# Kernel optimization log

Hardware: AMD Instinct MI355X
Metric: run time of the kernel (lower is better)

## Reference

```python
import jax, jax.numpy as jnp
import numpy as np

B, N, DIM = 8, 256, 256
INTER = DIM // 4          # downsample=4
POS_H = 64                # pos_mlp_hidden_dim
ATTN_H = INTER * 4        # attn_mlp_hidden_mult=4


def setup_inputs() -> dict:
    key = jax.random.key(0)
    ks = jax.random.split(key, 16)
    s = lambda fan_in: 1.0 / np.sqrt(fan_in)
    return {
        "x": jax.random.normal(ks[0], (B, N, DIM), jnp.float32),
        "y": jax.random.normal(ks[1], (B, N, DIM), jnp.float32),
        "x_pos": jax.random.normal(ks[2], (B, N, 3), jnp.float32),
        "y_pos": jax.random.normal(ks[3], (B, N, 3), jnp.float32),
        "mask": jax.random.randint(ks[4], (B, N), 0, 2) > 0,
        # linear weights stored (in, out) for direct matmul; torch Linear has no bias for g/theta/phi/conv_out
        "g_w": jax.random.normal(ks[5], (DIM, INTER), jnp.float32) * s(DIM),
        "theta_w": jax.random.normal(ks[6], (DIM, INTER), jnp.float32) * s(DIM),
        "phi_w": jax.random.normal(ks[7], (DIM, INTER), jnp.float32) * s(DIM),
        "pos_w1": jax.random.normal(ks[8], (3, POS_H), jnp.float32) * s(3),
        "pos_b1": jnp.zeros((POS_H,), jnp.float32),
        "pos_w2": jax.random.normal(ks[9], (POS_H, INTER), jnp.float32) * s(POS_H),
        "pos_b2": jnp.zeros((INTER,), jnp.float32),
        "attn_w1": jax.random.normal(ks[10], (INTER, ATTN_H), jnp.float32) * s(INTER),
        "attn_b1": jnp.zeros((ATTN_H,), jnp.float32),
        "attn_w2": jax.random.normal(ks[11], (ATTN_H, INTER), jnp.float32) * s(ATTN_H),
        "attn_b2": jnp.zeros((INTER,), jnp.float32),
        "out_w": jax.random.normal(ks[12], (INTER, DIM), jnp.float32) * s(INTER),
    }


def reference(x, y, x_pos, y_pos, mask, g_w, theta_w, phi_w,
              pos_w1, pos_b1, pos_w2, pos_b2,
              attn_w1, attn_b1, attn_w2, attn_b2, out_w):
    v = y @ g_w            # (b, j, d)
    q = x @ theta_w        # (b, i, d)
    k = y @ phi_w          # (b, j, d)
    # pairwise relative positions -> MLP embedding, (b, i, j, d)
    rel_pos = x_pos[:, :, None, :] - y_pos[:, None, :, :]
    rel_pos_emb = jax.nn.relu(rel_pos @ pos_w1 + pos_b1) @ pos_w2 + pos_b2
    # MLP-based attention score on (q_i - k_j + rel_pos_emb)
    qk_rel = q[:, :, None, :] - k[:, None, :, :]
    sim = jax.nn.relu((qk_rel + rel_pos_emb) @ attn_w1 + attn_b1) @ attn_w2 + attn_b2
    # masked softmax over j (dim=-2)
    pair_mask = mask[:, :, None] & mask[:, None, :]      # (b, i, j)
    neg = -jnp.finfo(sim.dtype).max
    sim = jnp.where(pair_mask[..., None], sim, neg)
    attn = jax.nn.softmax(sim, axis=-2)
    # value + positional embedding, then per-channel weighted aggregate over j
    v_full = v[:, None, :, :] + rel_pos_emb              # (b, i, j, d)
    agg = jnp.einsum('bijd,bijd->bid', attn, v_full)
    return x + agg @ out_w
```

## Files before the change

kernel.cpp:

```cpp
#include <hip/hip_runtime.h>
#include <hip/hip_bf16.h>

#define NB 8
#define NN 256
#define DIMV 256
#define DI 64
#define NEGMAX 3.402823466e+38f

typedef unsigned short u16;
typedef unsigned int u32;
typedef __attribute__((ext_vector_type(8))) short bf16x8;
typedef __attribute__((ext_vector_type(4))) float f32x4;
typedef __attribute__((ext_vector_type(2))) float f32x2;
typedef __attribute__((ext_vector_type(2))) unsigned int u32x2;

__device__ __forceinline__ u16 f2bf(float f) {
    __hip_bfloat16 h = __float2bfloat16(f);
    u16 u; __builtin_memcpy(&u, &h, 2); return u;
}
__device__ __forceinline__ u32 pack2(float a, float b) {
    return (u32)f2bf(a) | ((u32)f2bf(b) << 16);
}
__device__ __forceinline__ float ubf_lo(u32 u) {
    union { u32 u; float f; } x; x.u = u << 16; return x.f;
}
__device__ __forceinline__ float ubf_hi(u32 u) {
    union { u32 u; float f; } x; x.u = u & 0xffff0000u; return x.f;
}
__device__ __forceinline__ int fA(int row) { return ((row & 7) << 4) ^ ((row & 8) << 2); }
__device__ __forceinline__ int fB(int row) { return ((row >> 1) & 7) << 4; }

__global__ void prep_all(const float* __restrict__ x, const float* __restrict__ y,
                         const float* __restrict__ tw, const float* __restrict__ pw,
                         const float* __restrict__ gw,
                         const float* __restrict__ w1, const float* __restrict__ w2,
                         const float* __restrict__ pw2,
                         const float* __restrict__ pw1, const float* __restrict__ pb1,
                         float* __restrict__ q, float* __restrict__ k, float* __restrict__ v,
                         u16* __restrict__ w1s, u16* __restrict__ w2s,
                         u16* __restrict__ pw2s, u16* __restrict__ pw1f)
{
    __shared__ float xs[4][256];
    __shared__ float ys[4][256];
    const int blk = blockIdx.x;
    const int tid = threadIdx.x;

    if (blk >= 512) {
        const int idx = (blk - 512) * 256 + tid;
        const int e   = idx & 7;
        const int l   = (idx >> 3) & 63;
        const int l15 = l & 15, lh = l >> 4;
        {
            const int frag = idx >> 9;
            const int ks = frag & 1, c2 = (frag >> 1) & 1, hc = frag >> 2;
            w1s[idx] = f2bf(w1[(ks * 32 + lh * 8 + e) * 256 + hc * 32 + 2 * l15 + c2]);
        }
        {
            const int frag = idx >> 9;
            const int ct = frag & 3, hc = frag >> 2;
            w2s[idx] = f2bf(w2[(hc * 32 + lh * 8 + e) * 64 + 4 * l15 + ct]);
        }
        if (idx < 4096) {
            const int frag = idx >> 9;
            const int ks = frag & 1, ct = frag >> 1;
            pw2s[idx] = f2bf(pw2[(ks * 32 + lh * 8 + e) * 64 + 4 * l15 + ct]);
        }
        if (idx < 2048) {
            const int ct = idx >> 9;
            const int kk = lh * 8 + e;
            const int col = 4 * l15 + ct;
            float val = (kk < 3) ? pw1[kk * 64 + col] : ((kk == 3) ? pb1[col] : 0.f);
            pw1f[idx] = f2bf(val);
        }
        return;
    }

    const int b = blk >> 6;
    const int n0 = (blk & 63) * 4;
    {
        int r = tid >> 6, e = tid & 63;
        ((float4*)xs[r])[e] = ((const float4*)(x + (size_t)(b * NN + n0 + r) * DIMV))[e];
        ((float4*)ys[r])[e] = ((const float4*)(y + (size_t)(b * NN + n0 + r) * DIMV))[e];
    }
    __syncthreads();
    const int nl = tid >> 6, d = tid & 63;
    float aq = 0.f, ak = 0.f, av = 0.f;
    #pragma unroll 4
    for (int c = 0; c < 256; ++c) {
        float wq = tw[c * 64 + d], wk = pw[c * 64 + d], wv = gw[c * 64 + d];
        float xv = xs[nl][c], yv = ys[nl][c];
        aq += xv * wq; ak += yv * wk; av += yv * wv;
    }
    const int n = n0 + nl;
    q[(b * NN + n) * DI + d] = aq;
    k[(b * NN + n) * DI + d] = ak;
    v[(b * NN + n) * DI + d] = av;
}

__global__ __launch_bounds__(256, 2)
void fused_attn(const float* __restrict__ x, const float* __restrict__ x_pos,
                const float* __restrict__ y_pos, const int* __restrict__ mask,
                const float* __restrict__ pb2,
                const float* __restrict__ ab1, const float* __restrict__ ab2,
                const float* __restrict__ out_w,
                const float* __restrict__ qg, const float* __restrict__ kg,
                const float* __restrict__ vg,
                const u16* __restrict__ w1s, const u16* __restrict__ w2s,
                const u16* __restrict__ pw2s, const u16* __restrict__ pw1f,
                float* __restrict__ out)
{
    __shared__ __align__(16) char sT[4][8192];
    __shared__ __align__(16) char sHid[4][4096];
    __shared__ __align__(16) char sV2[4][4096];

    const int blk = blockIdx.x;
    const int b = blk >> 8;
    const int i = blk & 255;
    const int tid = threadIdx.x;
    const int l   = tid & 63;
    const int w   = tid >> 6;
    const int j0  = w * 64;
    const int l15 = l & 15;
    const int lh  = l >> 4;

    char* const sTw   = sT[w];
    char* const sHidw = sHid[w];
    char* const sV2w  = sV2[w];

    int stW[4], hcW[4];
    #pragma unroll
    for (int r = 0; r < 4; ++r) {
        const int lr = lh * 4 + r;
        stW[r] = (lr * 128 + l15 * 8) ^ fA(lr);
        hcW[r] = (lr * 64 + l15 * 4) ^ fB(lr);
    }
    const int stR0 = (l15 * 128 + lh * 16) ^ fA(l15);
    const int stR1 = stR0 ^ 64;
    const int hcR  = (l15 * 64 + lh * 16) ^ fB(l15);

    const int mjl = mask[b * NN + j0 + l];
    const unsigned long long mb = __ballot(mjl != 0);
    const bool mi_b = mask[b * NN + i] != 0;

    const float xp0 = x_pos[(b * NN + i) * 3 + 0];
    const float xp1 = x_pos[(b * NN + i) * 3 + 1];
    const float xp2 = x_pos[(b * NN + i) * 3 + 2];

    bf16x8 afr[4];
    #pragma unroll
    for (int rt = 0; rt < 4; ++rt) {
        const float* yp = y_pos + (size_t)(b * NN + j0 + rt * 16 + l15) * 3;
        const float r0 = xp0 - yp[0], r1 = xp1 - yp[1], r2 = xp2 - yp[2];
        union { u32 u[4]; bf16x8 v; } c;
        c.u[0] = (lh == 0) ? pack2(r0, r1) : 0u;
        c.u[1] = (lh == 0) ? pack2(r2, 1.0f) : 0u;
        c.u[2] = 0u; c.u[3] = 0u;
        afr[rt] = c.v;
    }
    bf16x8 pw1b[4];
    #pragma unroll
    for (int ct = 0; ct < 4; ++ct)
        pw1b[ct] = *(const bf16x8*)(pw1f + (ct * 64 + l) * 8);

    const f32x4 qv   = *(const f32x4*)&qg[((size_t)b * NN + i) * DI + 4 * l15];
    const f32x4 pb2v = *(const f32x4*)&pb2[4 * l15];
    bf16x8 bfr[4][2];
    #pragma unroll
    for (int ct = 0; ct < 4; ++ct)
        #pragma unroll
        for (int ks = 0; ks < 2; ++ks)
            bfr[ct][ks] = *(const bf16x8*)(pw2s + ((ct * 2 + ks) * 64 + l) * 8);

    f32x4 hA[4];
    #define HID_MFMA(RT)                                                        \
        { _Pragma("unroll") for (int ct = 0; ct < 4; ++ct) {                    \
            f32x4 z = {0.f, 0.f, 0.f, 0.f};                                     \
            hA[ct] = __builtin_amdgcn_mfma_f32_16x16x32_bf16(afr[RT], pw1b[ct], z, 0, 0, 0); } }
    #define HID_STORE(RT)                                                       \
        { char* hb = sHidw + (((RT) & 1) ? 2048 : 0);                           \
          _Pragma("unroll") for (int r = 0; r < 4; ++r) {                       \
            u32x2 hpk;                                                          \
            hpk[0] = pack2(fmaxf(hA[0][r], 0.f), fmaxf(hA[1][r], 0.f));         \
            hpk[1] = pack2(fmaxf(hA[2][r], 0.f), fmaxf(hA[3][r], 0.f));         \
            *(u32x2*)(hb + stW[r]) = hpk; } }

    u32x2 accVp[2][4];
    HID_MFMA(0);
    HID_STORE(0);
    #pragma unroll
    for (int rt = 0; rt < 4; ++rt) {
        if (rt < 3) { HID_MFMA(rt + 1); HID_STORE(rt + 1); }
        char* const hb = sHidw + ((rt & 1) ? 2048 : 0);
        const bf16x8 afc0 = *(const bf16x8*)(hb + stR0);
        const bf16x8 afc1 = *(const bf16x8*)(hb + stR1);

        f32x4 accR[4];
        #pragma unroll
        for (int ct = 0; ct < 4; ++ct) {
            f32x4 a = {pb2v[ct], pb2v[ct], pb2v[ct], pb2v[ct]};
            a = __builtin_amdgcn_mfma_f32_16x16x32_bf16(afc0, bfr[ct][0], a, 0, 0, 0);
            a = __builtin_amdgcn_mfma_f32_16x16x32_bf16(afc1, bfr[ct][1], a, 0, 0, 0);
            accR[ct] = a;
        }
        #pragma unroll
        for (int r = 0; r < 4; ++r) {
            const int row = j0 + rt * 16 + lh * 4 + r;
            const f32x4 kv = *(const f32x4*)&kg[((size_t)b * NN + row) * DI + 4 * l15];
            const f32x4 vv = *(const f32x4*)&vg[((size_t)b * NN + row) * DI + 4 * l15];
            float tv[4], vf[4];
            #pragma unroll
            for (int ct = 0; ct < 4; ++ct) {
                const float rpe = accR[ct][r];
                tv[ct] = qv[ct] - kv[ct] + rpe;
                vf[ct] = vv[ct] + rpe;
            }
            u32x2 tpk; tpk[0] = pack2(tv[0], tv[1]); tpk[1] = pack2(tv[2], tv[3]);
            u32x2 vpk; vpk[0] = pack2(vf[0], vf[1]); vpk[1] = pack2(vf[2], vf[3]);
            *(u32x2*)(sTw + stW[r] + rt * 2048) = tpk;
            if (rt < 2) accVp[rt][r] = vpk;
            else        *(u32x2*)(sV2w + stW[r] + (rt - 2) * 2048) = vpk;
        }
    }

    bf16x8 aT[4][2];
    #pragma unroll
    for (int rt = 0; rt < 4; ++rt) {
        aT[rt][0] = *(const bf16x8*)(sTw + stR0 + rt * 2048);
        aT[rt][1] = *(const bf16x8*)(sTw + stR1 + rt * 2048);
    }

    const f32x4 ab2v = *(const f32x4*)&ab2[4 * l15];
    f32x4 accS[4][4];
    #pragma unroll
    for (int rt = 0; rt < 4; ++rt)
        #pragma unroll
        for (int ct = 0; ct < 4; ++ct)
            accS[rt][ct] = (f32x4){ab2v[ct], ab2v[ct], ab2v[ct], ab2v[ct]};

    #pragma unroll
    for (int hc = 0; hc < 8; ++hc) {
        bf16x8 b1f[2][2];
        #pragma unroll
        for (int c2 = 0; c2 < 2; ++c2)
            #pragma unroll
            for (int ks = 0; ks < 2; ++ks)
                b1f[c2][ks] = *(const bf16x8*)(w1s + ((hc * 4 + c2 * 2 + ks) * 64 + l) * 8);
        bf16x8 b2f[4];
        #pragma unroll
        for (int ct = 0; ct < 4; ++ct)
            b2f[ct] = *(const bf16x8*)(w2s + ((hc * 4 + ct) * 64 + l) * 8);
        const f32x2 ab1v = *(const f32x2*)&ab1[hc * 32 + 2 * l15];
        const f32x4 ib0 = {ab1v[0], ab1v[0], ab1v[0], ab1v[0]};
        const f32x4 ib1 = {ab1v[1], ab1v[1], ab1v[1], ab1v[1]};
        __builtin_amdgcn_s_setprio(1);
        #pragma unroll
        for (int rt = 0; rt < 4; ++rt) {
            f32x4 h0 = ib0, h1 = ib1;
            h0 = __builtin_amdgcn_mfma_f32_16x16x32_bf16(aT[rt][0], b1f[0][0], h0, 0, 0, 0);
            h0 = __builtin_amdgcn_mfma_f32_16x16x32_bf16(aT[rt][1], b1f[0][1], h0, 0, 0, 0);
            h1 = __builtin_amdgcn_mfma_f32_16x16x32_bf16(aT[rt][0], b1f[1][0], h1, 0, 0, 0);
            h1 = __builtin_amdgcn_mfma_f32_16x16x32_bf16(aT[rt][1], b1f[1][1], h1, 0, 0, 0);
            #pragma unroll
            for (int r = 0; r < 4; ++r)
                *(u32*)(sHidw + hcW[r] + rt * 1024) =
                    pack2(fmaxf(h0[r], 0.f), fmaxf(h1[r], 0.f));
        }
        bf16x8 a2[4];
        #pragma unroll
        for (int rt = 0; rt < 4; ++rt)
            a2[rt] = *(const bf16x8*)(sHidw + hcR + rt * 1024);
        #pragma unroll
        for (int rt = 0; rt < 4; ++rt)
            #pragma unroll
            for (int ct = 0; ct < 4; ++ct)
                accS[rt][ct] = __builtin_amdgcn_mfma_f32_16x16x32_bf16(a2[rt], b2f[ct], accS[rt][ct], 0, 0, 0);
        __builtin_amdgcn_s_setprio(0);
    }

    float mx[4] = {-NEGMAX, -NEGMAX, -NEGMAX, -NEGMAX};
    #pragma unroll
    for (int rt = 0; rt < 4; ++rt)
        #pragma unroll
        for (int r = 0; r < 4; ++r) {
            const int ro = rt * 16 + lh * 4 + r;
            const bool bit = mi_b && ((mb >> ro) & 1ull);
            #pragma unroll
            for (int ct = 0; ct < 4; ++ct) {
                float s = bit ? accS[rt][ct][r] : -NEGMAX;
                accS[rt][ct][r] = s;
                mx[ct] = fmaxf(mx[ct], s);
            }
        }
    #pragma unroll
    for (int ct = 0; ct < 4; ++ct) {
        mx[ct] = fmaxf(mx[ct], __shfl_xor(mx[ct], 16));
        mx[ct] = fmaxf(mx[ct], __shfl_xor(mx[ct], 32));
    }
    float ssum[4] = {0.f, 0.f, 0.f, 0.f}, sagg[4] = {0.f, 0.f, 0.f, 0.f};
    #pragma unroll
    for (int rt = 0; rt < 4; ++rt)
        #pragma unroll
        for (int r = 0; r < 4; ++r) {
            u32x2 vpk;
            if (rt < 2) vpk = accVp[rt][r];
            else        vpk = *(const u32x2*)(sV2w + stW[r] + (rt - 2) * 2048);
            const float vfs[4] = {ubf_lo(vpk[0]), ubf_hi(vpk[0]), ubf_lo(vpk[1]), ubf_hi(vpk[1])};
            #pragma unroll
            for (int ct = 0; ct < 4; ++ct) {
                const float e = __expf(accS[rt][ct][r] - mx[ct]);
                ssum[ct] += e;
                sagg[ct] += e * vfs[ct];
            }
        }
    #pragma unroll
    for (int ct = 0; ct < 4; ++ct) {
        ssum[ct] += __shfl_xor(ssum[ct], 16);
        ssum[ct] += __shfl_xor(ssum[ct], 32);
        sagg[ct] += __shfl_xor(sagg[ct], 16);
        sagg[ct] += __shfl_xor(sagg[ct], 32);
    }
    {
        float* const redW = (float*)&sHid[w][0];
        if (lh == 0) {
            *(f32x4*)&redW[      4 * l15] = (f32x4){mx[0], mx[1], mx[2], mx[3]};
            *(f32x4*)&redW[ 64 + 4 * l15] = (f32x4){ssum[0], ssum[1], ssum[2], ssum[3]};
            *(f32x4*)&redW[128 + 4 * l15] = (f32x4){sagg[0], sagg[1], sagg[2], sagg[3]};
        }
    }
    __syncthreads();
    float* const redAll = (float*)&sHid[0][0];
    if (tid < 64) {
        const float m0 = redAll[tid],        m1 = redAll[1024 + tid],
                    m2 = redAll[2048 + tid], m3 = redAll[3072 + tid];
        const float M = fmaxf(fmaxf(m0, m1), fmaxf(m2, m3));
        const float e0 = __expf(m0 - M), e1 = __expf(m1 - M),
                    e2 = __expf(m2 - M), e3 = __expf(m3 - M);
        const float den = redAll[64 + tid] * e0 + redAll[1024 + 64 + tid] * e1
                        + redAll[2048 + 64 + tid] * e2 + redAll[3072 + 64 + tid] * e3;
        const float num = redAll[128 + tid] * e0 + redAll[1024 + 128 + tid] * e1
                        + redAll[2048 + 128 + tid] * e2 + redAll[3072 + 128 + tid] * e3;
        redAll[192 + tid] = num / den;
    }
    __syncthreads();

    {
        float acc = 0.f;
        #pragma unroll 16
        for (int d = 0; d < 64; ++d)
            acc += redAll[192 + d] * out_w[d * DIMV + tid];
        const int o = (b * NN + i) * DIMV + tid;
        out[o] = x[o] + acc;
    }
}

extern "C" void kernel_launch(void* const* d_in, const int* in_sizes, int n_in,
                              void* d_out, int out_size, void* d_ws, size_t ws_size,
                              hipStream_t stream)
{
    const float* x       = (const float*)d_in[0];
    const float* y       = (const float*)d_in[1];
    const float* x_pos   = (const float*)d_in[2];
    const float* y_pos   = (const float*)d_in[3];
    const int*   mask    = (const int*)d_in[4];
    const float* g_w     = (const float*)d_in[5];
    const float* theta_w = (const float*)d_in[6];
    const float* phi_w   = (const float*)d_in[7];
    const float* pos_w1  = (const float*)d_in[8];
    const float* pos_b1  = (const float*)d_in[9];
    const float* pos_w2  = (const float*)d_in[10];
    const float* pos_b2  = (const float*)d_in[11];
    const float* attn_w1 = (const float*)d_in[12];
    const float* attn_b1 = (const float*)d_in[13];
    const float* attn_w2 = (const float*)d_in[14];
    const float* attn_b2 = (const float*)d_in[15];
    const float* out_w   = (const float*)d_in[16];

    float* q = (float*)d_ws;
    float* k = q + NB * NN * DI;
    float* v = k + NB * NN * DI;
    u16* w1s  = (u16*)(v + NB * NN * DI);
    u16* w2s  = w1s + 16384;
    u16* pw2s = w2s + 16384;
    u16* pw1f = pw2s + 4096;

    prep_all<<<576, 256, 0, stream>>>(x, y, theta_w, phi_w, g_w,
                                      attn_w1, attn_w2, pos_w2, pos_w1, pos_b1,
                                      q, k, v, w1s, w2s, pw2s, pw1f);
    fused_attn<<<NB * NN, 256, 0, stream>>>(x, x_pos, y_pos, mask,
                                            pos_b2, attn_b1, attn_b2, out_w,
                                            q, k, v, w1s, w2s, pw2s, pw1f,
                                            (float*)d_out);
}
```

Baseline: 80.73 us.

## Double-buffer hidden-layer tiles to overlap first and second attention-MLP GEMMs

Software-pipelines the attention MLP hidden-chunk loop: the first GEMM plus ReLU for chunk hc+1 is computed and stored into an alternate LDS buffer while the second GEMM consumes chunk hc. The aim is to hide the LDS write-then-read dependency between the two MFMA stages. It reuses the sTw region as a ping-pong hidden buffer, which assumes sTw is large enough and that aT was already loaded into registers. The mask select is also recomputed in the exp loop instead of written back into accS.

New measurement: 82.25 us. About the same (+1.9%).

```diff
diff --git a/kernel.cpp b/kernel.cpp
--- a/kernel.cpp
+++ b/kernel.cpp
@@ -237,43 +237,41 @@
         for (int ct = 0; ct < 4; ++ct)
             accS[rt][ct] = (f32x4){ab2v[ct], ab2v[ct], ab2v[ct], ab2v[ct]};
 
+    #define G1_STORE(HC, BUF)                                                   \
+      { bf16x8 b1f[2][2];                                                       \
+        _Pragma("unroll") for (int c2 = 0; c2 < 2; ++c2)                        \
+          _Pragma("unroll") for (int ks = 0; ks < 2; ++ks)                      \
+            b1f[c2][ks] = *(const bf16x8*)(w1s + (((HC) * 4 + c2 * 2 + ks) * 64 + l) * 8); \
+        const f32x2 ab1v = *(const f32x2*)&ab1[(HC) * 32 + 2 * l15];            \
+        const f32x4 ib0 = {ab1v[0], ab1v[0], ab1v[0], ab1v[0]};                 \
+        const f32x4 ib1 = {ab1v[1], ab1v[1], ab1v[1], ab1v[1]};                 \
+        _Pragma("unroll") for (int rt = 0; rt < 4; ++rt) {                      \
+          f32x4 h0 = ib0, h1 = ib1;                                             \
+          h0 = __builtin_amdgcn_mfma_f32_16x16x32_bf16(aT[rt][0], b1f[0][0], h0, 0, 0, 0); \
+          h0 = __builtin_amdgcn_mfma_f32_16x16x32_bf16(aT[rt][1], b1f[0][1], h0, 0, 0, 0); \
+          h1 = __builtin_amdgcn_mfma_f32_16x16x32_bf16(aT[rt][0], b1f[1][0], h1, 0, 0, 0); \
+          h1 = __builtin_amdgcn_mfma_f32_16x16x32_bf16(aT[rt][1], b1f[1][1], h1, 0, 0, 0); \
+          _Pragma("unroll") for (int r = 0; r < 4; ++r)                         \
+            *(u32*)((BUF) + hcW[r] + rt * 1024) =                               \
+                pack2(fmaxf(h0[r], 0.f), fmaxf(h1[r], 0.f)); } }
+
+    #define G2_ACC(HC, BUF)                                                     \
+      { bf16x8 b2f[4];                                                          \
+        _Pragma("unroll") for (int ct = 0; ct < 4; ++ct)                        \
+          b2f[ct] = *(const bf16x8*)(w2s + (((HC) * 4 + ct) * 64 + l) * 8);     \
+        bf16x8 a2[4];                                                           \
+        _Pragma("unroll") for (int rt = 0; rt < 4; ++rt)                        \
+          a2[rt] = *(const bf16x8*)((BUF) + hcR + rt * 1024);                   \
+        _Pragma("unroll") for (int rt = 0; rt < 4; ++rt)                        \
+          _Pragma("unroll") for (int ct = 0; ct < 4; ++ct)                      \
+            accS[rt][ct] = __builtin_amdgcn_mfma_f32_16x16x32_bf16(a2[rt], b2f[ct], accS[rt][ct], 0, 0, 0); }
+
+    G1_STORE(0, sTw);
     #pragma unroll
     for (int hc = 0; hc < 8; ++hc) {
-        bf16x8 b1f[2][2];
-        #pragma unroll
-        for (int c2 = 0; c2 < 2; ++c2)
-            #pragma unroll
-            for (int ks = 0; ks < 2; ++ks)
-                b1f[c2][ks] = *(const bf16x8*)(w1s + ((hc * 4 + c2 * 2 + ks) * 64 + l) * 8);
-        bf16x8 b2f[4];
-        #pragma unroll
-        for (int ct = 0; ct < 4; ++ct)
-            b2f[ct] = *(const bf16x8*)(w2s + ((hc * 4 + ct) * 64 + l) * 8);
-        const f32x2 ab1v = *(const f32x2*)&ab1[hc * 32 + 2 * l15];
-        const f32x4 ib0 = {ab1v[0], ab1v[0], ab1v[0], ab1v[0]};
-        const f32x4 ib1 = {ab1v[1], ab1v[1], ab1v[1], ab1v[1]};
         __builtin_amdgcn_s_setprio(1);
-        #pragma unroll
-        for (int rt = 0; rt < 4; ++rt) {
-            f32x4 h0 = ib0, h1 = ib1;
-            h0 = __builtin_amdgcn_mfma_f32_16x16x32_bf16(aT[rt][0], b1f[0][0], h0, 0, 0, 0);
-            h0 = __builtin_amdgcn_mfma_f32_16x16x32_bf16(aT[rt][1], b1f[0][1], h0, 0, 0, 0);
-            h1 = __builtin_amdgcn_mfma_f32_16x16x32_bf16(aT[rt][0], b1f[1][0], h1, 0, 0, 0);
-            h1 = __builtin_amdgcn_mfma_f32_16x16x32_bf16(aT[rt][1], b1f[1][1], h1, 0, 0, 0);
-            #pragma unroll
-            for (int r = 0; r < 4; ++r)
-                *(u32*)(sHidw + hcW[r] + rt * 1024) =
-                    pack2(fmaxf(h0[r], 0.f), fmaxf(h1[r], 0.f));
-        }
-        bf16x8 a2[4];
-        #pragma unroll
-        for (int rt = 0; rt < 4; ++rt)
-            a2[rt] = *(const bf16x8*)(sHidw + hcR + rt * 1024);
-        #pragma unroll
-        for (int rt = 0; rt < 4; ++rt)
-            #pragma unroll
-            for (int ct = 0; ct < 4; ++ct)
-                accS[rt][ct] = __builtin_amdgcn_mfma_f32_16x16x32_bf16(a2[rt], b2f[ct], accS[rt][ct], 0, 0, 0);
+        if (hc < 7) { G1_STORE(hc + 1, sTw + (((hc + 1) & 1) ? 4096 : 0)); }
+        G2_ACC(hc, sTw + ((hc & 1) ? 4096 : 0));
         __builtin_amdgcn_s_setprio(0);
     }
 
@@ -286,8 +284,7 @@
             const bool bit = mi_b && ((mb >> ro) & 1ull);
             #pragma unroll
             for (int ct = 0; ct < 4; ++ct) {
-                float s = bit ? accS[rt][ct][r] : -NEGMAX;
-                accS[rt][ct][r] = s;
+                const float s = bit ? accS[rt][ct][r] : -NEGMAX;
                 mx[ct] = fmaxf(mx[ct], s);
             }
         }
@@ -301,13 +298,16 @@
     for (int rt = 0; rt < 4; ++rt)
         #pragma unroll
         for (int r = 0; r < 4; ++r) {
+            const int ro = rt * 16 + lh * 4 + r;
+            const bool bit = mi_b && ((mb >> ro) & 1ull);
             u32x2 vpk;
             if (rt < 2) vpk = accVp[rt][r];
             else        vpk = *(const u32x2*)(sV2w + stW[r] + (rt - 2) * 2048);
             const float vfs[4] = {ubf_lo(vpk[0]), ubf_hi(vpk[0]), ubf_lo(vpk[1]), ubf_hi(vpk[1])};
             #pragma unroll
             for (int ct = 0; ct < 4; ++ct) {
-                const float e = __expf(accS[rt][ct][r] - mx[ct]);
+                const float sm = bit ? accS[rt][ct][r] : -NEGMAX;
+                const float e = __expf(sm - mx[ct]);
                 ssum[ct] += e;
                 sagg[ct] += e * vfs[ct];
             }
```
